# Optimization experiments

Measured on AMD Instinct MI355X. Metric: run time of the kernel, lower is better.

## Reference

```python
import math
import jax, jax.numpy as jnp
import numpy as np

B, L, D, H = 2, 2048, 1024, 16
DK = D // H
N_TYPES = 6  # token types; < 3 => prompt (U/O/E), >= 3 => item (I)


def setup_inputs() -> dict:
    key = jax.random.key(0)
    ks = jax.random.split(key, 8)
    w_scale = 0.02
    return {
        "x": jax.random.normal(ks[0], (B, L, D), dtype=jnp.float32),
        "token_types": jax.random.randint(ks[1], (B, L), 0, N_TYPES, dtype=jnp.int32),
        "seq_lens": jax.random.randint(ks[2], (B,), L // 2, L + 1, dtype=jnp.int32),
        "W_q": jax.random.normal(ks[3], (D, D), dtype=jnp.float32) * w_scale,
        "W_k": jax.random.normal(ks[4], (D, D), dtype=jnp.float32) * w_scale,
        "W_v": jax.random.normal(ks[5], (D, D), dtype=jnp.float32) * w_scale,
        "W_u": jax.random.normal(ks[6], (D, D), dtype=jnp.float32) * w_scale,
        "W_o": jax.random.normal(ks[7], (D, D), dtype=jnp.float32) * w_scale,
    }


def reference(x, token_types, seq_lens, W_q, W_k, W_v, W_u, W_o):
    b, l, d = x.shape
    neg = jnp.finfo(x.dtype).min

    def proj(W):  # torch Linear (no bias): y = x @ W.T -> (b, H, l, dk)
        return jnp.einsum("bld,ed->ble", x, W).reshape(b, l, H, DK).transpose(0, 2, 1, 3)

    Q, K, V, U = proj(W_q), proj(W_k), proj(W_v), proj(W_u)

    scores = jnp.einsum("bhid,bhjd->bhij", Q, K) / math.sqrt(DK)  # (b,H,l,l)

    # Hybrid mask: causal (-inf above diagonal), but 0 wherever key j is a
    # prompt token (prompt<->prompt bidirectional, item->prompt allowed).
    is_prompt = token_types < 3                      # (b, l)
    causal = jnp.where(jnp.triu(jnp.ones((l, l), dtype=bool), k=1), neg, 0.0).astype(x.dtype)
    mask = jnp.where(is_prompt[:, None, :], jnp.asarray(0.0, x.dtype), causal[None, :, :])  # (b,l,l)
    scores = scores + mask[:, None, :, :]

    # Padding mask on key positions j >= seq_len
    pad = jnp.arange(l)[None, :] >= seq_lens[:, None]  # (b, l)
    scores = jnp.where(pad[:, None, None, :], neg, scores)

    attn = jax.nn.softmax(scores, axis=-1)
    out = jnp.einsum("bhij,bhjd->bhid", attn, V) * U   # HSTU pointwise gating
    out = out.transpose(0, 2, 1, 3).reshape(b, l, d)
    return jnp.einsum("bld,ed->ble", out, W_o)
```

## Files before the change

kernel.cpp:

```cpp
#include <hip/hip_runtime.h>


#define L_SEQ 2048

typedef __attribute__((ext_vector_type(8))) short bf16x8;
typedef __attribute__((ext_vector_type(8))) unsigned short u16x8;
typedef __attribute__((ext_vector_type(4))) float f32x4;
typedef __attribute__((ext_vector_type(16))) float f32x16;

#if __has_builtin(__builtin_amdgcn_exp2f)
#define EXP2F __builtin_amdgcn_exp2f
#else
#define EXP2F __builtin_exp2f
#endif

__device__ __forceinline__ unsigned short f2bf(float f) {
  union { float f; unsigned u; } c; c.f = f;
  unsigned r = c.u + 0x7FFFu + ((c.u >> 16) & 1u);
  return (unsigned short)(r >> 16);
}
__device__ __forceinline__ float bf2f(unsigned short h) {
  union { unsigned u; float f; } c; c.u = ((unsigned)h) << 16;
  return c.f;
}

__device__ __forceinline__ void async16(const void* g, void* l) {
  __builtin_amdgcn_global_load_lds((__attribute__((address_space(1))) void*)g,
                                   (__attribute__((address_space(3))) void*)l,
                                   16, 0, 0);
}

__device__ __forceinline__ unsigned cvtpk_bf16(float lo, float hi) {
  unsigned r; asm("v_cvt_pk_bf16_f32 %0, %1, %2" : "=v"(r) : "v"(lo), "v"(hi));
  return r;
}

__global__ __launch_bounds__(256) void cvt_all(
    const float* __restrict__ x,
    const float* __restrict__ wq, const float* __restrict__ wk,
    const float* __restrict__ wv, const float* __restrict__ wu,
    const float* __restrict__ wo,
    unsigned short* __restrict__ xb, unsigned short* __restrict__ wcat) {
  const int seg = blockIdx.x >> 10;
  const float* s;
  unsigned short* d;
  float sc = 1.0f;
  if (seg < 4)      { s = x + (size_t)seg * 1048576;  d = xb + (size_t)seg * 1048576; }
  else {
    const int ws = seg - 4;
    s = ws == 0 ? wq : ws == 1 ? wk : ws == 2 ? wv : ws == 3 ? wu : wo;
    d = wcat + (size_t)ws * 1048576;
    if (ws == 0) sc = 0.18033688011112042f;
  }
  const int i = ((blockIdx.x & 1023) * 256 + threadIdx.x) * 4;
  const float4 v = *reinterpret_cast<const float4*>(s + i);
  ushort4 o;
  o.x = f2bf(v.x * sc); o.y = f2bf(v.y * sc); o.z = f2bf(v.z * sc); o.w = f2bf(v.w * sc);
  *reinterpret_cast<ushort4*>(d + i) = o;
}

__global__ __launch_bounds__(64) void maskbuild(const int* __restrict__ tt,
                                                const int* __restrict__ sl,
                                                unsigned* __restrict__ allowed) {
  const int b = blockIdx.x >> 5, wv = blockIdx.x & 31;
  const int j = wv * 64 + threadIdx.x;
  const int seqlen = sl[b];
  const unsigned long long m = __ballot((tt[b * L_SEQ + j] < 3) && (j < seqlen));
  if (threadIdx.x == 0) {
    allowed[b * 64 + 2 * wv]     = (unsigned)m;
    allowed[b * 64 + 2 * wv + 1] = (unsigned)(m >> 32);
  }
}

__global__ __launch_bounds__(512, 2) void gemm256_bt(
    const unsigned short* __restrict__ A,
    const unsigned short* __restrict__ BT,
    unsigned short* __restrict__ Cb, int K)
{
  __shared__ char smem[131072];

  const int tid = threadIdx.x, w = tid >> 6, lane = tid & 63;
  const int lo = lane & 15, hi = lane >> 4;
  const int wm = w >> 2, wn = w & 3;
  const int d = blockIdx.x;
  const int lin = (d & 7) * 32 + (d >> 3);
  const int i0 = (lin >> 4) * 256, j0 = (lin & 15) * 256;

  const int rr = lane >> 3, ch = lane & 7;
  const int ksw = 8 * (ch ^ rr);

  auto stage = [&](int buf, int t) {
    const size_t k0 = (size_t)t * 64 + ksw;
    #pragma unroll
    for (int q = 0; q < 2; ++q) {
      const int p = 2 * w + q;
      const int row = 8 * p + rr;
      #pragma unroll
      for (int h = 0; h < 2; ++h) {
        async16(A  + (size_t)(i0 + h * 128 + row) * K + k0,
                smem + buf * 32768 + h * 16384 + p * 1024);
        async16(BT + (size_t)(j0 + h * 128 + row) * K + k0,
                smem + 65536 + buf * 32768 + h * 16384 + p * 1024);
      }
    }
  };

  f32x4 acc[8][4] = {};
  stage(0, 0);

  const int nt = K >> 6;
  for (int u = 0; u < nt; ++u) {
    const int buf = u & 1;
    if (u + 1 < nt) {
      stage(buf ^ 1, u + 1);
      asm volatile("s_waitcnt vmcnt(8)" ::: "memory");
    } else {
      asm volatile("s_waitcnt vmcnt(0)" ::: "memory");
    }
    __builtin_amdgcn_s_barrier();
    __builtin_amdgcn_sched_barrier(0);

    const char* Ah = smem + buf * 32768 + wm * 16384;
    const char* Bh = smem + 65536 + buf * 32768 + (wn >> 1) * 16384;
    const int brow0 = (wn & 1) * 64;

    bf16x8 bfr[4][2];
    #pragma unroll
    for (int n = 0; n < 4; ++n)
      #pragma unroll
      for (int ks = 0; ks < 2; ++ks)
        bfr[n][ks] = *reinterpret_cast<const bf16x8*>(
            Bh + (brow0 + n * 16 + lo) * 128 + 16 * ((ks * 4 + hi) ^ (lo & 7)));

    #pragma unroll
    for (int ph = 0; ph < 4; ++ph) {
      bf16x8 afr[2][2];
      #pragma unroll
      for (int mm = 0; mm < 2; ++mm)
        #pragma unroll
        for (int ks = 0; ks < 2; ++ks)
          afr[mm][ks] = *reinterpret_cast<const bf16x8*>(
              Ah + ((ph * 2 + mm) * 16 + lo) * 128 + 16 * ((ks * 4 + hi) ^ (lo & 7)));
      __builtin_amdgcn_s_barrier();
      __builtin_amdgcn_sched_barrier(0);
      __builtin_amdgcn_s_setprio(1);
      #pragma unroll
      for (int ks = 0; ks < 2; ++ks)
        #pragma unroll
        for (int mm = 0; mm < 2; ++mm)
          #pragma unroll
          for (int n = 0; n < 4; ++n)
            acc[ph * 2 + mm][n] = __builtin_amdgcn_mfma_f32_16x16x32_bf16(
                afr[mm][ks], bfr[n][ks], acc[ph * 2 + mm][n], 0, 0, 0);
      __builtin_amdgcn_s_setprio(0);
      __builtin_amdgcn_s_barrier();
      __builtin_amdgcn_sched_barrier(0);
    }
  }

  const int mi = (lin & 15) >> 2;
  const int cb0 = j0 & 1023;
  if (mi != 2) {
    unsigned short* base = Cb + (size_t)mi * 4194304;
    #pragma unroll
    for (int m = 0; m < 8; ++m) {
      const int row = i0 + wm * 128 + m * 16 + hi * 4;
      #pragma unroll
      for (int n = 0; n < 4; ++n) {
        const int col = cb0 + wn * 64 + n * 16 + lo;
        #pragma unroll
        for (int r = 0; r < 4; ++r)
          base[(size_t)(row + r) * 1024 + col] = f2bf(acc[m][n][r]);
      }
    }
  } else {
    #pragma unroll
    for (int m = 0; m < 8; ++m) {
      const int tl = (wm << 1) + (m >> 2);
      #pragma unroll
      for (int n = 0; n < 4; ++n) {
        const int dd = n * 16 + lo;
        char* ib = smem + (tl * 4 + wn) * 8192 + dd * 128;
        const int swd = dd & 7;
        #pragma unroll
        for (int r = 0; r < 4; ++r) {
          const int k = (m * 16 + hi * 4 + r) & 63;
          *(unsigned short*)(ib + 16 * ((k >> 3) ^ swd) + 2 * (k & 7)) =
              f2bf(acc[m][n][r]);
        }
      }
    }
    __builtin_amdgcn_s_barrier();
    unsigned short* V = Cb + (size_t)2 * 4194304;
    const int bI = i0 >> 11;
    const int t0 = (i0 & 2047) >> 6;
    const int h0 = cb0 >> 6;
    #pragma unroll
    for (int img = 0; img < 16; ++img) {
      const int tl = img >> 2, hl = img & 3;
      const size_t ob = ((size_t)(bI * 16 + h0 + hl) * 32 + (t0 + tl)) * 4096;
      *reinterpret_cast<u16x8*>(V + ob + tid * 8) =
          *reinterpret_cast<const u16x8*>(smem + img * 8192 + tid * 16);
    }
  }
}

template<int OUT_BF16, int MF>
__global__ __launch_bounds__(256) void gemm_bt(
    const unsigned short* __restrict__ A,
    const unsigned short* __restrict__ BT,
    float* __restrict__ Cf, unsigned short* __restrict__ Cb,
    int M, int N, int K, int cpx, int nbxm, int nbxs)
{
  __shared__ unsigned short As[2][MF * 32 * 32];
  __shared__ unsigned short Bs[2][128 * 32];

  const int tid = threadIdx.x;
  const int w = tid >> 6, lane = tid & 63;
  const int lo = lane & 15, hi = lane >> 4;
  const int d = blockIdx.x + gridDim.x * blockIdx.y;
  const int lin = (d & 7) * cpx + (d >> 3);
  const int i0 = (lin >> nbxs) * (MF * 32), j0 = (lin & nbxm) * 128;
  const int wr = w >> 1, wc = w & 1;
  const int rsub = lane >> 2, csub = (lane & 3) * 8;

  f32x4 acc[MF][4] = {};

  auto stage = [&](int buf, int k0) {
    #pragma unroll
    for (int q = 0; q < 2; ++q) {
      const int cB = w * 2 + q;
      async16(BT + (size_t)(j0 + cB * 16 + rsub) * K + k0 + csub, &Bs[buf][cB * 512]);
      if (q < MF / 2) {
        const int cA = w * (MF / 2) + q;
        async16(A + (size_t)(i0 + cA * 16 + rsub) * K + k0 + csub, &As[buf][cA * 512]);
      }
    }
  };

  stage(0, 0);
  __syncthreads();

  const int nt = K >> 5;
  for (int t = 0; t < nt; ++t) {
    const int buf = t & 1;
    if (t + 1 < nt) stage(buf ^ 1, (t + 1) << 5);
    bf16x8 a[MF], b[4];
    #pragma unroll
    for (int m = 0; m < MF; ++m)
      a[m] = *reinterpret_cast<const bf16x8*>(
          &As[buf][(wr * (MF * 16) + m * 16 + lo) * 32 + hi * 8]);
    #pragma unroll
    for (int n = 0; n < 4; ++n)
      b[n] = *reinterpret_cast<const bf16x8*>(&Bs[buf][(wc * 64 + n * 16 + lo) * 32 + hi * 8]);
    #pragma unroll
    for (int m = 0; m < MF; ++m)
      #pragma unroll
      for (int n = 0; n < 4; ++n)
        acc[m][n] = __builtin_amdgcn_mfma_f32_16x16x32_bf16(a[m], b[n], acc[m][n], 0, 0, 0);
    __syncthreads();
  }

  #pragma unroll
  for (int m = 0; m < MF; ++m) {
    const int row = i0 + wr * (MF * 16) + m * 16 + hi * 4;
    #pragma unroll
    for (int n = 0; n < 4; ++n) {
      const int col = j0 + wc * 64 + n * 16 + lo;
      #pragma unroll
      for (int r = 0; r < 4; ++r) {
        if (OUT_BF16) Cb[(size_t)(row + r) * N + col] = f2bf(acc[m][n][r]);
        else          Cf[(size_t)(row + r) * N + col] = acc[m][n][r];
      }
    }
  }
}

__global__ __launch_bounds__(512, 4) void hstu_attn(
    const unsigned short* __restrict__ qm,
    const unsigned short* __restrict__ km,
    const unsigned short* __restrict__ vimg,
    const unsigned short* __restrict__ um,
    const unsigned* __restrict__ allowed,
    const int* __restrict__ slens,
    unsigned short* __restrict__ gated)
{
  __shared__ char smem[65536];

  const int dlin = blockIdx.x + (blockIdx.y << 4) + (blockIdx.z << 8);
  const int lin = ((dlin & 7) << 6) | (dlin >> 3);
  const int qt = lin & 15, h = (lin >> 4) & 15, b = lin >> 8;
  const int i0 = qt * 128;
  const int tid = threadIdx.x, w = tid >> 6, lane = tid & 63;
  const int g = w >> 2, wq = w & 3;
  const int c = lane & 31, sb = lane >> 5;
  const int seqlen = slens[b];
  const size_t rbm = (size_t)b * L_SEQ * 1024;
  const size_t vb = (size_t)(b * 16 + h) * 32 * 4096;
  const int qrow = i0 + wq * 32 + c;

  auto stageK = [&](int buf, int t) {
    const int j0 = t * 64;
    char* Kb = smem + (g * 2 + buf) * 8192;
    #pragma unroll
    for (int q = 0; q < 2; ++q) {
      const int p = wq * 2 + q;
      const int krow = 8 * p + (lane >> 3);
      const int d0 = 8 * ((lane & 7) ^ (lane >> 3));
      async16(km + rbm + (size_t)(j0 + krow) * 1024 + h * 64 + d0, Kb + p * 1024);
    }
  };
  auto stageV = [&](int buf, int t) {
    char* Vb = smem + 32768 + (g * 2 + buf) * 8192;
    #pragma unroll
    for (int q = 0; q < 2; ++q) {
      const int p = wq * 2 + q;
      async16(vimg + vb + (size_t)t * 4096 + p * 512 + lane * 8, Vb + p * 1024);
    }
  };

  const int nt = (seqlen + 63) >> 6;
  const int niter = (nt + 1) >> 1;

  stageK(0, g); stageV(0, g);

  bf16x8 qf[4];
  #pragma unroll
  for (int kd = 0; kd < 4; ++kd)
    qf[kd] = *reinterpret_cast<const bf16x8*>(
        qm + rbm + (size_t)qrow * 1024 + h * 64 + kd * 16 + sb * 8);
  const unsigned pmword = allowed[b * 64 + lane];
  const int limb = (qrow < seqlen - 1 ? qrow : seqlen - 1) - 4 * sb;

  union { unsigned u[4]; bf16x8 v; } one_;
  one_.u[0] = one_.u[1] = one_.u[2] = one_.u[3] = 0x3F803F80u;
  const bf16x8 onesv = one_.v;

  f32x16 o0 = {}, o1 = {}, ls = {};

  asm volatile("s_waitcnt vmcnt(0)" ::: "memory");
  __builtin_amdgcn_s_barrier();
  __builtin_amdgcn_sched_barrier(0);

  for (int i = 0; i < niter; ++i) {
    const int t = 2 * i + g;
    const bool active = t < nt;
    const int buf = i & 1;
    const int j0 = t * 64;
    const bool pre = (t + 2 < nt);

    if (active) {
      if (pre) { stageK(buf ^ 1, t + 2); stageV(buf ^ 1, t + 2); }

      const char* Kb = smem + (g * 2 + buf) * 8192;
      const char* Vb = smem + 32768 + (g * 2 + buf) * 8192;
      const bool fast = (j0 + 64 <= seqlen) && (j0 + 63 <= i0 + wq * 32);

      #pragma unroll
      for (int z = 0; z < 2; ++z) {
        f32x16 s = {};
        __builtin_amdgcn_s_setprio(1);
        #pragma unroll
        for (int kd = 0; kd < 4; ++kd) {
          const bf16x8 kf = *reinterpret_cast<const bf16x8*>(
              Kb + (32 * z + c) * 128 + (((2 * kd + sb) ^ (c & 7)) << 4));
          s = __builtin_amdgcn_mfma_f32_32x32x16_bf16(kf, qf[kd], s, 0, 0, 0);
        }
        __builtin_amdgcn_s_setprio(0);

        if (fast) {
          #pragma unroll
          for (int r = 0; r < 16; ++r) s[r] = EXP2F(s[r]);
        } else {
          const unsigned pmz = __builtin_amdgcn_readlane(pmword, 2 * t + z);
          const int lim = limb - j0 - 32 * z;
          const unsigned cm = lim < 0 ? 0u : (lim >= 31 ? ~0u : ((2u << lim) - 1u));
          const unsigned al = (pmz >> (4 * sb)) | cm;
          #pragma unroll
          for (int r = 0; r < 16; ++r) {
            const int kc = (r & 3) + 8 * (r >> 2);
            const float p = EXP2F(s[r]);
            s[r] = ((al >> kc) & 1) ? p : 0.f;
          }
        }

        unsigned U0, U1, W0, W1;
        U0 = cvtpk_bf16(s[0], s[1]);  U1 = cvtpk_bf16(s[2], s[3]);
        W0 = cvtpk_bf16(s[4], s[5]);  W1 = cvtpk_bf16(s[6], s[7]);
        asm("v_permlane32_swap_b32 %0, %1" : "+v"(U0), "+v"(W0));
        asm("v_permlane32_swap_b32 %0, %1" : "+v"(U1), "+v"(W1));
        union { unsigned u[4]; bf16x8 v; } pu;
        pu.u[0] = U0; pu.u[1] = U1; pu.u[2] = W0; pu.u[3] = W1;
        const bf16x8 pfE = pu.v;
        U0 = cvtpk_bf16(s[8], s[9]);   U1 = cvtpk_bf16(s[10], s[11]);
        W0 = cvtpk_bf16(s[12], s[13]); W1 = cvtpk_bf16(s[14], s[15]);
        asm("v_permlane32_swap_b32 %0, %1" : "+v"(U0), "+v"(W0));
        asm("v_permlane32_swap_b32 %0, %1" : "+v"(U1), "+v"(W1));
        pu.u[0] = U0; pu.u[1] = U1; pu.u[2] = W0; pu.u[3] = W1;
        const bf16x8 pfO = pu.v;

        const int kpE = 2 * z, kpO = 2 * z + 1;
        const int swE = ((2 * kpE + sb) ^ (c & 7)) << 4;
        const int swO = ((2 * kpO + sb) ^ (c & 7)) << 4;
        const bf16x8 ve0 = *reinterpret_cast<const bf16x8*>(Vb + c * 128 + swE);
        const bf16x8 ve1 = *reinterpret_cast<const bf16x8*>(Vb + (32 + c) * 128 + swE);
        const bf16x8 vo0 = *reinterpret_cast<const bf16x8*>(Vb + c * 128 + swO);
        const bf16x8 vo1 = *reinterpret_cast<const bf16x8*>(Vb + (32 + c) * 128 + swO);
        __builtin_amdgcn_s_setprio(1);
        o0 = __builtin_amdgcn_mfma_f32_32x32x16_bf16(ve0, pfE, o0, 0, 0, 0);
        o1 = __builtin_amdgcn_mfma_f32_32x32x16_bf16(ve1, pfE, o1, 0, 0, 0);
        ls = __builtin_amdgcn_mfma_f32_32x32x16_bf16(onesv, pfE, ls, 0, 0, 0);
        o0 = __builtin_amdgcn_mfma_f32_32x32x16_bf16(vo0, pfO, o0, 0, 0, 0);
        o1 = __builtin_amdgcn_mfma_f32_32x32x16_bf16(vo1, pfO, o1, 0, 0, 0);
        ls = __builtin_amdgcn_mfma_f32_32x32x16_bf16(onesv, pfO, ls, 0, 0, 0);
        __builtin_amdgcn_s_setprio(0);
      }
      asm volatile("s_waitcnt vmcnt(0)" ::: "memory");
    }
    __builtin_amdgcn_s_barrier();
    __builtin_amdgcn_sched_barrier(0);
  }

  const float lsum = ls[0];

  float* cb = (float*)smem;
  const int col = wq * 64 + lane;
  if (g == 1) {
    #pragma unroll
    for (int r = 0; r < 16; ++r) {
      cb[r * 260 + col]        = o0[r];
      cb[(16 + r) * 260 + col] = o1[r];
    }
    cb[32 * 260 + col] = lsum;
  }
  __syncthreads();
  if (g == 1) return;
  #pragma unroll
  for (int r = 0; r < 16; ++r) {
    o0[r] += cb[r * 260 + col];
    o1[r] += cb[(16 + r) * 260 + col];
  }
  const float rin = 1.0f / (lsum + cb[32 * 260 + col]);

  #pragma unroll
  for (int n = 0; n < 2; ++n) {
    const f32x16 o = n ? o1 : o0;
    #pragma unroll
    for (int rq = 0; rq < 4; ++rq) {
      const int d0 = n * 32 + 8 * rq + 4 * sb;
      const ushort4 uu = *reinterpret_cast<const ushort4*>(
          um + rbm + (size_t)qrow * 1024 + h * 64 + d0);
      ushort4 gg;
      gg.x = f2bf(o[4 * rq + 0] * rin * bf2f(uu.x));
      gg.y = f2bf(o[4 * rq + 1] * rin * bf2f(uu.y));
      gg.z = f2bf(o[4 * rq + 2] * rin * bf2f(uu.z));
      gg.w = f2bf(o[4 * rq + 3] * rin * bf2f(uu.w));
      *reinterpret_cast<ushort4*>(
          gated + (size_t)(b * L_SEQ + qrow) * 1024 + h * 64 + d0) = gg;
    }
  }
}

extern "C" void kernel_launch(void* const* d_in, const int* in_sizes, int n_in,
                              void* d_out, int out_size, void* d_ws, size_t ws_size,
                              hipStream_t stream) {
  const float* x  = (const float*)d_in[0];
  const int* tt   = (const int*)d_in[1];
  const int* sl   = (const int*)d_in[2];
  const float* Wq = (const float*)d_in[3];
  const float* Wk = (const float*)d_in[4];
  const float* Wv = (const float*)d_in[5];
  const float* Wu = (const float*)d_in[6];
  const float* Wo = (const float*)d_in[7];
  float* out = (float*)d_out;

  unsigned* allowed     = (unsigned*)d_ws;
  unsigned short* xb    = (unsigned short*)d_ws + 256;
  unsigned short* wcat  = xb    + (size_t)4096 * 1024;
  unsigned short* wob   = wcat  + (size_t)4096 * 1024;
  unsigned short* qkvu  = wob   + (size_t)1024 * 1024;
  unsigned short* gated = qkvu  + (size_t)4096 * 4096;

  cvt_all<<<9216, 256, 0, stream>>>(x, Wq, Wk, Wv, Wu, Wo, xb, wcat);

  gemm256_bt<<<256, 512, 0, stream>>>(xb, wcat, qkvu, 1024);

  maskbuild<<<64, 64, 0, stream>>>(tt, sl, allowed);

  hstu_attn<<<dim3(16, 16, 2), 512, 0, stream>>>(
      qkvu, qkvu + (size_t)4194304, qkvu + (size_t)2 * 4194304,
      qkvu + (size_t)3 * 4194304, allowed, sl, gated);

  gemm_bt<0, 2><<<dim3(8, 64), 256, 0, stream>>>(gated, wob, out, nullptr,
                                                 4096, 1024, 1024, 64, 7, 3);
}
```

Before: 120.5 us.

## Software-pipeline QK and PV with triple-buffered K and replace ones-MFMA row sums

Triple-buffers K tiles and double-buffers V tiles per wave group so the next tile's QK MFMAs are issued before the current tile's exp and PV work, overlapping matrix and vector phases. The row-sum MFMA against a ones vector is removed; instead each lane accumulates probabilities in a scalar and combines halves with a cross-lane shuffle. LDS use grows from 64KB to 80KB per block, which may reduce occupancy under the declared launch bounds, and the extra live score registers add register pressure.

```diff
diff --git a/kernel.cpp b/kernel.cpp
--- a/kernel.cpp
+++ b/kernel.cpp
@@ -285,7 +285,7 @@
     const int* __restrict__ slens,
     unsigned short* __restrict__ gated)
 {
-  __shared__ char smem[65536];
+  __shared__ char smem[81920];
 
   const int dlin = blockIdx.x + (blockIdx.y << 4) + (blockIdx.z << 8);
   const int lin = ((dlin & 7) << 6) | (dlin >> 3);
@@ -299,9 +299,15 @@
   const size_t vb = (size_t)(b * 16 + h) * 32 * 4096;
   const int qrow = i0 + wq * 32 + c;
 
-  auto stageK = [&](int buf, int t) {
+  char* const gbase = smem + g * 40960;
+  char* kb0 = gbase;
+  char* kb1 = gbase + 8192;
+  char* kb2 = gbase + 16384;
+  char* vb0 = gbase + 24576;
+  char* vb1 = gbase + 32768;
+
+  auto stageK = [&](char* Kb, int t) {
     const int j0 = t * 64;
-    char* Kb = smem + (g * 2 + buf) * 8192;
     #pragma unroll
     for (int q = 0; q < 2; ++q) {
       const int p = wq * 2 + q;
@@ -310,8 +316,7 @@
       async16(km + rbm + (size_t)(j0 + krow) * 1024 + h * 64 + d0, Kb + p * 1024);
     }
   };
-  auto stageV = [&](int buf, int t) {
-    char* Vb = smem + 32768 + (g * 2 + buf) * 8192;
+  auto stageV = [&](char* Vb, int t) {
     #pragma unroll
     for (int q = 0; q < 2; ++q) {
       const int p = wq * 2 + q;
@@ -321,8 +326,9 @@
 
   const int nt = (seqlen + 63) >> 6;
   const int niter = (nt + 1) >> 1;
-
-  stageK(0, g); stageV(0, g);
+  const int myn = (nt - g + 1) >> 1;
+
+  stageK(kb0, g); stageK(kb1, g + 2); stageV(vb0, g);
 
   bf16x8 qf[4];
   #pragma unroll
@@ -332,96 +338,101 @@
   const unsigned pmword = allowed[b * 64 + lane];
   const int limb = (qrow < seqlen - 1 ? qrow : seqlen - 1) - 4 * sb;
 
-  union { unsigned u[4]; bf16x8 v; } one_;
-  one_.u[0] = one_.u[1] = one_.u[2] = one_.u[3] = 0x3F803F80u;
-  const bf16x8 onesv = one_.v;
-
-  f32x16 o0 = {}, o1 = {}, ls = {};
+  f32x16 o0 = {}, o1 = {};
+  float rs = 0.f;
+
+  auto QK = [&](const char* Kb, int z) {
+    f32x16 s = {};
+    __builtin_amdgcn_s_setprio(1);
+    #pragma unroll
+    for (int kd = 0; kd < 4; ++kd) {
+      const bf16x8 kf = *reinterpret_cast<const bf16x8*>(
+          Kb + (32 * z + c) * 128 + (((2 * kd + sb) ^ (c & 7)) << 4));
+      s = __builtin_amdgcn_mfma_f32_32x32x16_bf16(kf, qf[kd], s, 0, 0, 0);
+    }
+    __builtin_amdgcn_s_setprio(0);
+    return s;
+  };
+
+  auto FINISH = [&](f32x16 s, int t, int z, const char* Vb) {
+    const int j0 = t * 64;
+    const bool fast = (j0 + 64 <= seqlen) && (j0 + 63 <= i0 + wq * 32);
+    if (fast) {
+      #pragma unroll
+      for (int r = 0; r < 16; ++r) { s[r] = EXP2F(s[r]); rs += s[r]; }
+    } else {
+      const unsigned pmz = __builtin_amdgcn_readlane(pmword, 2 * t + z);
+      const int lim = limb - j0 - 32 * z;
+      const unsigned cm = lim < 0 ? 0u : (lim >= 31 ? ~0u : ((2u << lim) - 1u));
+      const unsigned al = (pmz >> (4 * sb)) | cm;
+      #pragma unroll
+      for (int r = 0; r < 16; ++r) {
+        const int kc = (r & 3) + 8 * (r >> 2);
+        const float p = EXP2F(s[r]);
+        s[r] = ((al >> kc) & 1) ? p : 0.f;
+        rs += s[r];
+      }
+    }
+
+    unsigned U0, U1, W0, W1;
+    U0 = cvtpk_bf16(s[0], s[1]);  U1 = cvtpk_bf16(s[2], s[3]);
+    W0 = cvtpk_bf16(s[4], s[5]);  W1 = cvtpk_bf16(s[6], s[7]);
+    asm("v_permlane32_swap_b32 %0, %1" : "+v"(U0), "+v"(W0));
+    asm("v_permlane32_swap_b32 %0, %1" : "+v"(U1), "+v"(W1));
+    union { unsigned u[4]; bf16x8 v; } pu;
+    pu.u[0] = U0; pu.u[1] = U1; pu.u[2] = W0; pu.u[3] = W1;
+    const bf16x8 pfE = pu.v;
+    U0 = cvtpk_bf16(s[8], s[9]);   U1 = cvtpk_bf16(s[10], s[11]);
+    W0 = cvtpk_bf16(s[12], s[13]); W1 = cvtpk_bf16(s[14], s[15]);
+    asm("v_permlane32_swap_b32 %0, %1" : "+v"(U0), "+v"(W0));
+    asm("v_permlane32_swap_b32 %0, %1" : "+v"(U1), "+v"(W1));
+    pu.u[0] = U0; pu.u[1] = U1; pu.u[2] = W0; pu.u[3] = W1;
+    const bf16x8 pfO = pu.v;
+
+    const int kpE = 2 * z, kpO = 2 * z + 1;
+    const int swE = ((2 * kpE + sb) ^ (c & 7)) << 4;
+    const int swO = ((2 * kpO + sb) ^ (c & 7)) << 4;
+    const bf16x8 ve0 = *reinterpret_cast<const bf16x8*>(Vb + c * 128 + swE);
+    const bf16x8 ve1 = *reinterpret_cast<const bf16x8*>(Vb + (32 + c) * 128 + swE);
+    const bf16x8 vo0 = *reinterpret_cast<const bf16x8*>(Vb + c * 128 + swO);
+    const bf16x8 vo1 = *reinterpret_cast<const bf16x8*>(Vb + (32 + c) * 128 + swO);
+    __builtin_amdgcn_s_setprio(1);
+    o0 = __builtin_amdgcn_mfma_f32_32x32x16_bf16(ve0, pfE, o0, 0, 0, 0);
+    o1 = __builtin_amdgcn_mfma_f32_32x32x16_bf16(ve1, pfE, o1, 0, 0, 0);
+    o0 = __builtin_amdgcn_mfma_f32_32x32x16_bf16(vo0, pfO, o0, 0, 0, 0);
+    o1 = __builtin_amdgcn_mfma_f32_32x32x16_bf16(vo1, pfO, o1, 0, 0, 0);
+    __builtin_amdgcn_s_setprio(0);
+  };
 
   asm volatile("s_waitcnt vmcnt(0)" ::: "memory");
   __builtin_amdgcn_s_barrier();
   __builtin_amdgcn_sched_barrier(0);
 
+  f32x16 sE = QK(kb0, 0);
+  f32x16 sO;
+
   for (int i = 0; i < niter; ++i) {
-    const int t = 2 * i + g;
-    const bool active = t < nt;
-    const int buf = i & 1;
-    const int j0 = t * 64;
-    const bool pre = (t + 2 < nt);
-
-    if (active) {
-      if (pre) { stageK(buf ^ 1, t + 2); stageV(buf ^ 1, t + 2); }
-
-      const char* Kb = smem + (g * 2 + buf) * 8192;
-      const char* Vb = smem + 32768 + (g * 2 + buf) * 8192;
-      const bool fast = (j0 + 64 <= seqlen) && (j0 + 63 <= i0 + wq * 32);
-
-      #pragma unroll
-      for (int z = 0; z < 2; ++z) {
-        f32x16 s = {};
-        __builtin_amdgcn_s_setprio(1);
-        #pragma unroll
-        for (int kd = 0; kd < 4; ++kd) {
-          const bf16x8 kf = *reinterpret_cast<const bf16x8*>(
-              Kb + (32 * z + c) * 128 + (((2 * kd + sb) ^ (c & 7)) << 4));
-          s = __builtin_amdgcn_mfma_f32_32x32x16_bf16(kf, qf[kd], s, 0, 0, 0);
-        }
-        __builtin_amdgcn_s_setprio(0);
-
-        if (fast) {
-          #pragma unroll
-          for (int r = 0; r < 16; ++r) s[r] = EXP2F(s[r]);
-        } else {
-          const unsigned pmz = __builtin_amdgcn_readlane(pmword, 2 * t + z);
-          const int lim = limb - j0 - 32 * z;
-          const unsigned cm = lim < 0 ? 0u : (lim >= 31 ? ~0u : ((2u << lim) - 1u));
-          const unsigned al = (pmz >> (4 * sb)) | cm;
-          #pragma unroll
-          for (int r = 0; r < 16; ++r) {
-            const int kc = (r & 3) + 8 * (r >> 2);
-            const float p = EXP2F(s[r]);
-            s[r] = ((al >> kc) & 1) ? p : 0.f;
-          }
-        }
-
-        unsigned U0, U1, W0, W1;
-        U0 = cvtpk_bf16(s[0], s[1]);  U1 = cvtpk_bf16(s[2], s[3]);
-        W0 = cvtpk_bf16(s[4], s[5]);  W1 = cvtpk_bf16(s[6], s[7]);
-        asm("v_permlane32_swap_b32 %0, %1" : "+v"(U0), "+v"(W0));
-        asm("v_permlane32_swap_b32 %0, %1" : "+v"(U1), "+v"(W1));
-        union { unsigned u[4]; bf16x8 v; } pu;
-        pu.u[0] = U0; pu.u[1] = U1; pu.u[2] = W0; pu.u[3] = W1;
-        const bf16x8 pfE = pu.v;
-        U0 = cvtpk_bf16(s[8], s[9]);   U1 = cvtpk_bf16(s[10], s[11]);
-        W0 = cvtpk_bf16(s[12], s[13]); W1 = cvtpk_bf16(s[14], s[15]);
-        asm("v_permlane32_swap_b32 %0, %1" : "+v"(U0), "+v"(W0));
-        asm("v_permlane32_swap_b32 %0, %1" : "+v"(U1), "+v"(W1));
-        pu.u[0] = U0; pu.u[1] = U1; pu.u[2] = W0; pu.u[3] = W1;
-        const bf16x8 pfO = pu.v;
-
-        const int kpE = 2 * z, kpO = 2 * z + 1;
-        const int swE = ((2 * kpE + sb) ^ (c & 7)) << 4;
-        const int swO = ((2 * kpO + sb) ^ (c & 7)) << 4;
-        const bf16x8 ve0 = *reinterpret_cast<const bf16x8*>(Vb + c * 128 + swE);
-        const bf16x8 ve1 = *reinterpret_cast<const bf16x8*>(Vb + (32 + c) * 128 + swE);
-        const bf16x8 vo0 = *reinterpret_cast<const bf16x8*>(Vb + c * 128 + swO);
-        const bf16x8 vo1 = *reinterpret_cast<const bf16x8*>(Vb + (32 + c) * 128 + swO);
-        __builtin_amdgcn_s_setprio(1);
-        o0 = __builtin_amdgcn_mfma_f32_32x32x16_bf16(ve0, pfE, o0, 0, 0, 0);
-        o1 = __builtin_amdgcn_mfma_f32_32x32x16_bf16(ve1, pfE, o1, 0, 0, 0);
-        ls = __builtin_amdgcn_mfma_f32_32x32x16_bf16(onesv, pfE, ls, 0, 0, 0);
-        o0 = __builtin_amdgcn_mfma_f32_32x32x16_bf16(vo0, pfO, o0, 0, 0, 0);
-        o1 = __builtin_amdgcn_mfma_f32_32x32x16_bf16(vo1, pfO, o1, 0, 0, 0);
-        ls = __builtin_amdgcn_mfma_f32_32x32x16_bf16(onesv, pfO, ls, 0, 0, 0);
-        __builtin_amdgcn_s_setprio(0);
-      }
+    const bool act = i < myn;
+    if (act) {
+      const int t = 2 * i + g;
+      if (i + 1 < myn) stageV(vb1, t + 2);
+      if (i + 2 < myn) stageK(kb2, t + 4);
+
+      sO = QK(kb0, 1);
+      FINISH(sE, t, 0, vb0);
+
+      if (i + 1 < myn) sE = QK(kb1, 0);
+      FINISH(sO, t, 1, vb0);
+
       asm volatile("s_waitcnt vmcnt(0)" ::: "memory");
     }
     __builtin_amdgcn_s_barrier();
     __builtin_amdgcn_sched_barrier(0);
-  }
-
-  const float lsum = ls[0];
+    char* tk = kb0; kb0 = kb1; kb1 = kb2; kb2 = tk;
+    char* tv = vb0; vb0 = vb1; vb1 = tv;
+  }
+
+  const float lsum = rs + __shfl_xor(rs, 32, 64);
 
   float* cb = (float*)smem;
   const int col = wq * 64 + lane;
```

After: 152.6 us. 26.7% more time.

## Fuse mask build into convert kernel and drop ones-MFMA row-sum in attention

Applied to the files above, without the earlier changes.

The mask-building kernel is folded into the conversion kernel as extra blocks, which removes one launch. In the attention loop, the row sum is now accumulated in fp32 on the VALU instead of through an extra MFMA against a ones vector, and the halves are combined with a cross-lane shuffle at the end. The QK^T step now issues both 32-key sub-tiles' MFMAs interleaved before any softmax work, to expose more independent matrix ops. This trades matrix-core work for VALU adds and raises register pressure. The sum now uses unrounded fp32 probabilities rather than their bf16-rounded values.

```diff
diff --git a/kernel.cpp b/kernel.cpp
--- a/kernel.cpp
+++ b/kernel.cpp
@@ -40,7 +40,22 @@
     const float* __restrict__ wq, const float* __restrict__ wk,
     const float* __restrict__ wv, const float* __restrict__ wu,
     const float* __restrict__ wo,
-    unsigned short* __restrict__ xb, unsigned short* __restrict__ wcat) {
+    unsigned short* __restrict__ xb, unsigned short* __restrict__ wcat,
+    const int* __restrict__ tt, const int* __restrict__ sl,
+    unsigned* __restrict__ allowed) {
+  if (blockIdx.x >= 9216) {
+    const int k = blockIdx.x - 9216;
+    const int wv64 = (k << 2) + (threadIdx.x >> 6);
+    const int b = wv64 >> 5, w32 = wv64 & 31;
+    const int lane = threadIdx.x & 63;
+    const int j = w32 * 64 + lane;
+    const unsigned long long m = __ballot((tt[b * L_SEQ + j] < 3) && (j < sl[b]));
+    if (lane == 0) {
+      allowed[b * 64 + 2 * w32]     = (unsigned)m;
+      allowed[b * 64 + 2 * w32 + 1] = (unsigned)(m >> 32);
+    }
+    return;
+  }
   const int seg = blockIdx.x >> 10;
   const float* s;
   unsigned short* d;
@@ -59,19 +74,6 @@
   *reinterpret_cast<ushort4*>(d + i) = o;
 }
 
-__global__ __launch_bounds__(64) void maskbuild(const int* __restrict__ tt,
-                                                const int* __restrict__ sl,
-                                                unsigned* __restrict__ allowed) {
-  const int b = blockIdx.x >> 5, wv = blockIdx.x & 31;
-  const int j = wv * 64 + threadIdx.x;
-  const int seqlen = sl[b];
-  const unsigned long long m = __ballot((tt[b * L_SEQ + j] < 3) && (j < seqlen));
-  if (threadIdx.x == 0) {
-    allowed[b * 64 + 2 * wv]     = (unsigned)m;
-    allowed[b * 64 + 2 * wv + 1] = (unsigned)(m >> 32);
-  }
-}
-
 __global__ __launch_bounds__(512, 2) void gemm256_bt(
     const unsigned short* __restrict__ A,
     const unsigned short* __restrict__ BT,
@@ -276,6 +278,52 @@
   }
 }
 
+#define FINZ(SS, ZZ)                                                          \
+  {                                                                           \
+    if (fast) {                                                               \
+      _Pragma("unroll")                                                       \
+      for (int r = 0; r < 16; ++r) { SS[r] = EXP2F(SS[r]); rs += SS[r]; }     \
+    } else {                                                                  \
+      const unsigned pmz = __builtin_amdgcn_readlane(pmword, 2 * t + ZZ);     \
+      const int lim = limb - j0 - 32 * ZZ;                                    \
+      const unsigned cm = lim < 0 ? 0u : (lim >= 31 ? ~0u : ((2u << lim) - 1u)); \
+      const unsigned al = (pmz >> (4 * sb)) | cm;                             \
+      _Pragma("unroll")                                                       \
+      for (int r = 0; r < 16; ++r) {                                          \
+        const int kc = (r & 3) + 8 * (r >> 2);                                \
+        const float p = EXP2F(SS[r]);                                         \
+        SS[r] = ((al >> kc) & 1) ? p : 0.f;                                   \
+        rs += SS[r];                                                          \
+      }                                                                       \
+    }                                                                         \
+    unsigned U0, U1, W0, W1;                                                  \
+    U0 = cvtpk_bf16(SS[0], SS[1]);  U1 = cvtpk_bf16(SS[2], SS[3]);            \
+    W0 = cvtpk_bf16(SS[4], SS[5]);  W1 = cvtpk_bf16(SS[6], SS[7]);            \
+    asm("v_permlane32_swap_b32 %0, %1" : "+v"(U0), "+v"(W0));                 \
+    asm("v_permlane32_swap_b32 %0, %1" : "+v"(U1), "+v"(W1));                 \
+    union { unsigned u[4]; bf16x8 v; } pu;                                    \
+    pu.u[0] = U0; pu.u[1] = U1; pu.u[2] = W0; pu.u[3] = W1;                   \
+    const bf16x8 pfA = pu.v;                                                  \
+    U0 = cvtpk_bf16(SS[8], SS[9]);   U1 = cvtpk_bf16(SS[10], SS[11]);         \
+    W0 = cvtpk_bf16(SS[12], SS[13]); W1 = cvtpk_bf16(SS[14], SS[15]);         \
+    asm("v_permlane32_swap_b32 %0, %1" : "+v"(U0), "+v"(W0));                 \
+    asm("v_permlane32_swap_b32 %0, %1" : "+v"(U1), "+v"(W1));                 \
+    pu.u[0] = U0; pu.u[1] = U1; pu.u[2] = W0; pu.u[3] = W1;                   \
+    const bf16x8 pfB = pu.v;                                                  \
+    const int swA = ((4 * ZZ + sb) ^ (c & 7)) << 4;                           \
+    const int swB = ((4 * ZZ + 2 + sb) ^ (c & 7)) << 4;                       \
+    const bf16x8 va0 = *reinterpret_cast<const bf16x8*>(Vb + c * 128 + swA);  \
+    const bf16x8 va1 = *reinterpret_cast<const bf16x8*>(Vb + (32 + c) * 128 + swA); \
+    const bf16x8 vb0 = *reinterpret_cast<const bf16x8*>(Vb + c * 128 + swB);  \
+    const bf16x8 vb1 = *reinterpret_cast<const bf16x8*>(Vb + (32 + c) * 128 + swB); \
+    __builtin_amdgcn_s_setprio(1);                                            \
+    o0 = __builtin_amdgcn_mfma_f32_32x32x16_bf16(va0, pfA, o0, 0, 0, 0);      \
+    o1 = __builtin_amdgcn_mfma_f32_32x32x16_bf16(va1, pfA, o1, 0, 0, 0);      \
+    o0 = __builtin_amdgcn_mfma_f32_32x32x16_bf16(vb0, pfB, o0, 0, 0, 0);      \
+    o1 = __builtin_amdgcn_mfma_f32_32x32x16_bf16(vb1, pfB, o1, 0, 0, 0);      \
+    __builtin_amdgcn_s_setprio(0);                                            \
+  }
+
 __global__ __launch_bounds__(512, 4) void hstu_attn(
     const unsigned short* __restrict__ qm,
     const unsigned short* __restrict__ km,
@@ -296,7 +344,7 @@
   const int c = lane & 31, sb = lane >> 5;
   const int seqlen = slens[b];
   const size_t rbm = (size_t)b * L_SEQ * 1024;
-  const size_t vb = (size_t)(b * 16 + h) * 32 * 4096;
+  const size_t vbg = (size_t)(b * 16 + h) * 32 * 4096;
   const int qrow = i0 + wq * 32 + c;
 
   auto stageK = [&](int buf, int t) {
@@ -315,7 +363,7 @@
     #pragma unroll
     for (int q = 0; q < 2; ++q) {
       const int p = wq * 2 + q;
-      async16(vimg + vb + (size_t)t * 4096 + p * 512 + lane * 8, Vb + p * 1024);
+      async16(vimg + vbg + (size_t)t * 4096 + p * 512 + lane * 8, Vb + p * 1024);
     }
   };
 
@@ -332,11 +380,8 @@
   const unsigned pmword = allowed[b * 64 + lane];
   const int limb = (qrow < seqlen - 1 ? qrow : seqlen - 1) - 4 * sb;
 
-  union { unsigned u[4]; bf16x8 v; } one_;
-  one_.u[0] = one_.u[1] = one_.u[2] = one_.u[3] = 0x3F803F80u;
-  const bf16x8 onesv = one_.v;
-
-  f32x16 o0 = {}, o1 = {}, ls = {};
+  f32x16 o0 = {}, o1 = {};
+  float rs = 0.f;
 
   asm volatile("s_waitcnt vmcnt(0)" ::: "memory");
   __builtin_amdgcn_s_barrier();
@@ -356,72 +401,28 @@
       const char* Vb = smem + 32768 + (g * 2 + buf) * 8192;
       const bool fast = (j0 + 64 <= seqlen) && (j0 + 63 <= i0 + wq * 32);
 
-      #pragma unroll
-      for (int z = 0; z < 2; ++z) {
-        f32x16 s = {};
-        __builtin_amdgcn_s_setprio(1);
-        #pragma unroll
-        for (int kd = 0; kd < 4; ++kd) {
-          const bf16x8 kf = *reinterpret_cast<const bf16x8*>(
-              Kb + (32 * z + c) * 128 + (((2 * kd + sb) ^ (c & 7)) << 4));
-          s = __builtin_amdgcn_mfma_f32_32x32x16_bf16(kf, qf[kd], s, 0, 0, 0);
-        }
-        __builtin_amdgcn_s_setprio(0);
-
-        if (fast) {
-          #pragma unroll
-          for (int r = 0; r < 16; ++r) s[r] = EXP2F(s[r]);
-        } else {
-          const unsigned pmz = __builtin_amdgcn_readlane(pmword, 2 * t + z);
-          const int lim = limb - j0 - 32 * z;
-          const unsigned cm = lim < 0 ? 0u : (lim >= 31 ? ~0u : ((2u << lim) - 1u));
-          const unsigned al = (pmz >> (4 * sb)) | cm;
-          #pragma unroll
-          for (int r = 0; r < 16; ++r) {
-            const int kc = (r & 3) + 8 * (r >> 2);
-            const float p = EXP2F(s[r]);
-            s[r] = ((al >> kc) & 1) ? p : 0.f;
-          }
-        }
-
-        unsigned U0, U1, W0, W1;
-        U0 = cvtpk_bf16(s[0], s[1]);  U1 = cvtpk_bf16(s[2], s[3]);
-        W0 = cvtpk_bf16(s[4], s[5]);  W1 = cvtpk_bf16(s[6], s[7]);
-        asm("v_permlane32_swap_b32 %0, %1" : "+v"(U0), "+v"(W0));
-        asm("v_permlane32_swap_b32 %0, %1" : "+v"(U1), "+v"(W1));
-        union { unsigned u[4]; bf16x8 v; } pu;
-        pu.u[0] = U0; pu.u[1] = U1; pu.u[2] = W0; pu.u[3] = W1;
-        const bf16x8 pfE = pu.v;
-        U0 = cvtpk_bf16(s[8], s[9]);   U1 = cvtpk_bf16(s[10], s[11]);
-        W0 = cvtpk_bf16(s[12], s[13]); W1 = cvtpk_bf16(s[14], s[15]);
-        asm("v_permlane32_swap_b32 %0, %1" : "+v"(U0), "+v"(W0));
-        asm("v_permlane32_swap_b32 %0, %1" : "+v"(U1), "+v"(W1));
-        pu.u[0] = U0; pu.u[1] = U1; pu.u[2] = W0; pu.u[3] = W1;
-        const bf16x8 pfO = pu.v;
-
-        const int kpE = 2 * z, kpO = 2 * z + 1;
-        const int swE = ((2 * kpE + sb) ^ (c & 7)) << 4;
-        const int swO = ((2 * kpO + sb) ^ (c & 7)) << 4;
-        const bf16x8 ve0 = *reinterpret_cast<const bf16x8*>(Vb + c * 128 + swE);
-        const bf16x8 ve1 = *reinterpret_cast<const bf16x8*>(Vb + (32 + c) * 128 + swE);
-        const bf16x8 vo0 = *reinterpret_cast<const bf16x8*>(Vb + c * 128 + swO);
-        const bf16x8 vo1 = *reinterpret_cast<const bf16x8*>(Vb + (32 + c) * 128 + swO);
-        __builtin_amdgcn_s_setprio(1);
-        o0 = __builtin_amdgcn_mfma_f32_32x32x16_bf16(ve0, pfE, o0, 0, 0, 0);
-        o1 = __builtin_amdgcn_mfma_f32_32x32x16_bf16(ve1, pfE, o1, 0, 0, 0);
-        ls = __builtin_amdgcn_mfma_f32_32x32x16_bf16(onesv, pfE, ls, 0, 0, 0);
-        o0 = __builtin_amdgcn_mfma_f32_32x32x16_bf16(vo0, pfO, o0, 0, 0, 0);
-        o1 = __builtin_amdgcn_mfma_f32_32x32x16_bf16(vo1, pfO, o1, 0, 0, 0);
-        ls = __builtin_amdgcn_mfma_f32_32x32x16_bf16(onesv, pfO, ls, 0, 0, 0);
-        __builtin_amdgcn_s_setprio(0);
-      }
+      f32x16 sE = {}, sO = {};
+      __builtin_amdgcn_s_setprio(1);
+      #pragma unroll
+      for (int kd = 0; kd < 4; ++kd) {
+        const int sw = ((2 * kd + sb) ^ (c & 7)) << 4;
+        const bf16x8 kfE = *reinterpret_cast<const bf16x8*>(Kb + c * 128 + sw);
+        const bf16x8 kfO = *reinterpret_cast<const bf16x8*>(Kb + (32 + c) * 128 + sw);
+        sE = __builtin_amdgcn_mfma_f32_32x32x16_bf16(kfE, qf[kd], sE, 0, 0, 0);
+        sO = __builtin_amdgcn_mfma_f32_32x32x16_bf16(kfO, qf[kd], sO, 0, 0, 0);
+      }
+      __builtin_amdgcn_s_setprio(0);
+
+      FINZ(sE, 0)
+      FINZ(sO, 1)
+
       asm volatile("s_waitcnt vmcnt(0)" ::: "memory");
     }
     __builtin_amdgcn_s_barrier();
     __builtin_amdgcn_sched_barrier(0);
   }
 
-  const float lsum = ls[0];
+  const float lsum = rs + __shfl_xor(rs, 32, 64);
 
   float* cb = (float*)smem;
   const int col = wq * 64 + lane;
@@ -481,11 +482,10 @@
   unsigned short* qkvu  = wob   + (size_t)1024 * 1024;
   unsigned short* gated = qkvu  + (size_t)4096 * 4096;
 
-  cvt_all<<<9216, 256, 0, stream>>>(x, Wq, Wk, Wv, Wu, Wo, xb, wcat);
+  cvt_all<<<9232, 256, 0, stream>>>(x, Wq, Wk, Wv, Wu, Wo, xb, wcat,
+                                    tt, sl, allowed);
 
   gemm256_bt<<<256, 512, 0, stream>>>(xb, wcat, qkvu, 1024);
-
-  maskbuild<<<64, 64, 0, stream>>>(tt, sl, allowed);
 
   hstu_attn<<<dim3(16, 16, 2), 512, 0, stream>>>(
       qkvu, qkvu + (size_t)4194304, qkvu + (size_t)2 * 4194304,
```

New measurement: 118.1 us. 1.02x faster.
